# Optimization experiments

Hardware: AMD Instinct MI355X
Metric: run time of the kernel (lower is better)

Reference implementation:

```python
import jax, jax.numpy as jnp
import numpy as np

B, N, FEAT, D = 8, 2048, 64, 6
RADIUS, NSAMPLE, TOPK, NHEAD, NLAYER = 0.3, 64, 16, 8, 2
EPS = 1e-5


def _bn(x, p, axis=1):
    # eval-mode batchnorm; p rows = (gamma, beta, running_mean, running_var)
    g, b, m, v = p
    sh = [1] * x.ndim
    sh[axis] = -1
    rs = lambda t: t.reshape(sh)
    return (x - rs(m)) * (rs(g) / jnp.sqrt(rs(v) + EPS)) + rs(b)


def _ln(x, g, b):
    mu = jnp.mean(x, -1, keepdims=True)
    var = jnp.mean((x - mu) ** 2, -1, keepdims=True)
    return (x - mu) / jnp.sqrt(var + EPS) * g + b


def _mha(x, w_in, b_in, w_out, b_out):
    bsz, n, e = x.shape
    hd = e // NHEAD
    qkv = x @ w_in.T + b_in                      # [B,N,3E]
    q, k, v = jnp.split(qkv, 3, axis=-1)
    sp = lambda t: t.reshape(bsz, n, NHEAD, hd).transpose(0, 2, 1, 3)  # [B,H,N,hd]
    q, k, v = sp(q), sp(k), sp(v)
    att = jax.nn.softmax(jnp.einsum('bhnd,bhmd->bhnm', q, k) * (1.0 / hd ** 0.5), axis=-1)
    o = jnp.einsum('bhnm,bhmd->bhnd', att, v).transpose(0, 2, 1, 3).reshape(bsz, n, e)
    return o @ w_out.T + b_out


def _forward(sortvec, input, tl_win, tl_bin, tl_wout, tl_bout, tl_w1, tl_b1, tl_w2, tl_b2,
             tl_ln1g, tl_ln1b, tl_ln2g, tl_ln2b,
             fg_w0, fg_b0, fg_w1, fg_b1, fg_w2, fg_b2, fbn0, fbn1, fbn2,
             rc_w0, rc_b0, rc_w1, rc_b1, rc_w2, rc_b2, rbn0, rbn1, rbn2,
             fl_w0, fl_b0, fl_w1, fl_b1, lbn0, lbn1):
    b = sortvec.shape[0]
    n = sortvec.shape[-1]
    relu = jax.nn.relu

    # --- input self-attention (2 post-norm TransformerEncoder layers) ---
    x = sortvec[:, 0].transpose(0, 2, 1)         # [B,N,FEAT]
    for l in range(NLAYER):
        a = _mha(x, tl_win[l], tl_bin[l], tl_wout[l], tl_bout[l])
        x = _ln(x + a, tl_ln1g[l], tl_ln1b[l])
        f = relu(x @ tl_w1[l].T + tl_b1[l]) @ tl_w2[l].T + tl_b2[l]
        x = _ln(x + f, tl_ln2g[l], tl_ln2b[l])

    # --- feat_generator (RFFNet: Conv2d(FEAT,1) then 1x1 convs) + BN + relu ---
    s = jnp.einsum('cf,bnf->bcn', fg_w0, x) + fg_b0[:, None]   # [B,64,N]
    s = relu(_bn(s, fbn0))
    s = relu(_bn(jnp.einsum('co,bon->bcn', fg_w1, s) + fg_b1[:, None], fbn1))
    s = relu(_bn(jnp.einsum('co,bon->bcn', fg_w2, s) + fg_b2[:, None], fbn2))
    scores = s[:, 0]                              # [B,N]

    # --- top-k point selection ---
    _, idx = jax.lax.top_k(scores, TOPK)          # [B,K]
    all_points = input.transpose(0, 2, 1)         # [B,N,6]
    bidx = jnp.arange(b)[:, None]
    query = all_points[bidx, idx]                 # [B,K,6]

    # --- query_ball_point (PointNet++ style) ---
    xyz, qxyz = all_points[..., :3], query[..., :3]
    sqr = jnp.sum((qxyz[:, :, None, :] - xyz[:, None, :, :]) ** 2, -1)   # [B,K,N]
    gidx = jnp.where(sqr > RADIUS ** 2, n, jnp.arange(n)[None, None, :])
    gidx = jnp.sort(gidx, axis=-1)[..., :NSAMPLE]                        # [B,K,S]
    gidx = jnp.where(gidx == n, gidx[..., :1], gidx)
    radius_points = all_points[jnp.arange(b)[:, None, None], gidx]       # [B,K,S,6]
    grouped = jnp.concatenate([query[:, :, None, :], radius_points], axis=2)  # [B,K,S+1,6]

    # --- radius_cnn (Conv3d (1,S+1,6) then 1x1x1) + BN3d + relu ---
    r = jnp.einsum('cpd,bkpd->bck', rc_w0, grouped) + rc_b0[:, None]     # [B,128,K]
    r = relu(_bn(r, rbn0))
    r = relu(_bn(jnp.einsum('co,bok->bck', rc_w1, r) + rc_b1[:, None], rbn1))
    r = relu(_bn(jnp.einsum('co,bok->bck', rc_w2, r) + rc_b2[:, None], rbn2))  # [B,512,K]

    # --- flatten + Linear/BN1d/relu chain ---
    h = r.reshape(b, -1)                          # [B, 512*K]
    h = relu(_bn(h @ fl_w0.T + fl_b0, lbn0))
    h = relu(_bn(h @ fl_w1.T + fl_b1, lbn1))
    return h[..., None], idx                      # [B,512,1], [B,K]


def setup_inputs() -> dict:
    key = jax.random.key(0)
    ks = iter(jax.random.split(key, 80))
    rnd = lambda shape, s=0.02: jax.random.normal(next(ks), shape, jnp.float32) * s

    def bn_p(c):
        g = 1.0 + rnd((c,))
        bb = rnd((c,))
        m = rnd((c,))
        v = 1.0 + 0.1 * jnp.abs(rnd((c,), 1.0))
        return jnp.stack([g, bb, m, v])

    F = FEAT
    return dict(
        sortvec=jax.random.normal(next(ks), (B, 1, F, N), jnp.float32),
        input=jax.random.normal(next(ks), (B, D, N), jnp.float32),
        tl_win=rnd((NLAYER, 3 * F, F)), tl_bin=rnd((NLAYER, 3 * F)),
        tl_wout=rnd((NLAYER, F, F)), tl_bout=rnd((NLAYER, F)),
        tl_w1=rnd((NLAYER, 2048, F)), tl_b1=rnd((NLAYER, 2048)),
        tl_w2=rnd((NLAYER, F, 2048)), tl_b2=rnd((NLAYER, F)),
        tl_ln1g=jnp.ones((NLAYER, F)), tl_ln1b=jnp.zeros((NLAYER, F)),
        tl_ln2g=jnp.ones((NLAYER, F)), tl_ln2b=jnp.zeros((NLAYER, F)),
        fg_w0=rnd((64, F), 0.1), fg_b0=jnp.zeros((64,)),
        fg_w1=rnd((16, 64), 0.1), fg_b1=jnp.zeros((16,)),
        fg_w2=rnd((1, 16), 0.1), fg_b2=jnp.zeros((1,)),
        fbn0=bn_p(64), fbn1=bn_p(16), fbn2=bn_p(1),
        rc_w0=rnd((128, NSAMPLE + 1, D), 0.05), rc_b0=jnp.zeros((128,)),
        rc_w1=rnd((256, 128), 0.05), rc_b1=jnp.zeros((256,)),
        rc_w2=rnd((512, 256), 0.05), rc_b2=jnp.zeros((512,)),
        rbn0=bn_p(128), rbn1=bn_p(256), rbn2=bn_p(512),
        fl_w0=rnd((1024, 512 * TOPK), 0.02), fl_b0=jnp.zeros((1024,)),
        fl_w1=rnd((512, 1024), 0.02), fl_b1=jnp.zeros((512,)),
        lbn0=bn_p(1024), lbn1=bn_p(512),
    )


def reference(sortvec, input, tl_win, tl_bin, tl_wout, tl_bout, tl_w1, tl_b1, tl_w2, tl_b2,
              tl_ln1g, tl_ln1b, tl_ln2g, tl_ln2b,
              fg_w0, fg_b0, fg_w1, fg_b1, fg_w2, fg_b2, fbn0, fbn1, fbn2,
              rc_w0, rc_b0, rc_w1, rc_b1, rc_w2, rc_b2, rbn0, rbn1, rbn2,
              fl_w0, fl_b0, fl_w1, fl_b1, lbn0, lbn1):
    return _forward(sortvec, input, tl_win, tl_bin, tl_wout, tl_bout, tl_w1, tl_b1, tl_w2, tl_b2,
                    tl_ln1g, tl_ln1b, tl_ln2g, tl_ln2b,
                    fg_w0, fg_b0, fg_w1, fg_b1, fg_w2, fg_b2, fbn0, fbn1, fbn2,
                    rc_w0, rc_b0, rc_w1, rc_b1, rc_w2, rc_b2, rbn0, rbn1, rbn2,
                    fl_w0, fl_b0, fl_w1, fl_b1, lbn0, lbn1)
```

## Files before the change

kernel.cpp:

```cpp
#include <hip/hip_runtime.h>
#include <hip/hip_bf16.h>
#include <math.h>

#define BB 8
#define NN 2048
#define FF 64
#define DD 6
#define NSAMP 64
#define TOPK 16
#define NHEAD 8
#define HD 8
#define NLAYER 2
#define EPSF 1e-5f
#define R2 0.09f

typedef short short8 __attribute__((ext_vector_type(8)));
typedef float f32x4 __attribute__((ext_vector_type(4)));
typedef unsigned uint4v __attribute__((ext_vector_type(4)));
typedef unsigned int u32;

__device__ inline unsigned pk2(float x) {
  unsigned b = __float_as_uint(x);
  unsigned hi = (b + 0x7fffu + ((b >> 16) & 1u)) >> 16;
  float r = x - __uint_as_float(hi << 16);
  unsigned c = __float_as_uint(r);
  unsigned lo = (c + 0x7fffu + ((c >> 16) & 1u)) >> 16;
  return (hi << 16) | lo;
}

__device__ inline unsigned short bf16r(float x) {
  unsigned b = __float_as_uint(x);
  return (unsigned short)((b + 0x7fffu + ((b >> 16) & 1u)) >> 16);
}

__device__ __forceinline__ void gl16(const void* g, void* l) {
  __builtin_amdgcn_global_load_lds((const __attribute__((address_space(1))) u32*)g,
                                   (__attribute__((address_space(3))) u32*)l, 16, 0, 0);
}

__global__ void k_transpose(const float* __restrict__ sv, float* __restrict__ x) {
  int i = blockIdx.x * 256 + threadIdx.x;
  if (i >= BB * NN * FF) return;
  int f = i % FF;
  int n = (i / FF) % NN;
  int b = i / (FF * NN);
  x[i] = sv[(b * FF + f) * NN + n];
}

__global__ void k_wimg(const float* __restrict__ w1, const float* __restrict__ w2,
                       unsigned short* __restrict__ img) {
  int i = blockIdx.x * 256 + threadIdx.x;
  int e = i & 4095;
  int plane = (i >> 12) & 3;
  int chg = (i >> 14) & 31;
  int l = i >> 19;
  int r = e >> 6, sh = (e >> 3) & 7, inner = e & 7;
  int s = sh ^ (r & 7);
  float v;
  if (plane < 2) v = w1[((size_t)(l * 2048 + chg * 64 + r)) * 64 + s * 8 + inner];
  else           v = w2[((size_t)(l * 64 + r)) * 2048 + chg * 64 + s * 8 + inner];
  unsigned p = pk2(v);
  img[i] = (unsigned short)((plane & 1) ? (p & 0xffffu) : (p >> 16));
}

__global__ void k_qkv3(const float* __restrict__ x, const float* __restrict__ win,
                       const float* __restrict__ bin, float* __restrict__ qbuf,
                       uint4* __restrict__ kp4, uint4* __restrict__ vp4) {
  __shared__ float xs[64 * 68];
  __shared__ float ws[64 * 68];
  int row0 = blockIdx.x * 64, y = blockIdx.y, col0 = y * 64;
  int t = threadIdx.x;
  #pragma unroll
  for (int i = 0; i < 4; ++i) {
    int q = t + i * 256, r = q >> 4, c = (q & 15) * 4;
    *(float4*)(xs + r * 68 + c) = *(const float4*)(x + (size_t)(row0 + r) * 64 + c);
    *(float4*)(ws + r * 68 + c) = *(const float4*)(win + (size_t)(col0 + r) * 64 + c);
  }
  __syncthreads();
  int tx = t & 15, ty = t >> 4;
  float acc[4][4] = {};
  for (int f = 0; f < 64; f += 4) {
    float4 xv[4], wv[4];
    #pragma unroll
    for (int ri = 0; ri < 4; ++ri) xv[ri] = *(const float4*)(xs + (ty * 4 + ri) * 68 + f);
    #pragma unroll
    for (int ci = 0; ci < 4; ++ci) wv[ci] = *(const float4*)(ws + (tx + 16 * ci) * 68 + f);
    #pragma unroll
    for (int ri = 0; ri < 4; ++ri)
      #pragma unroll
      for (int ci = 0; ci < 4; ++ci)
        acc[ri][ci] += xv[ri].x * wv[ci].x + xv[ri].y * wv[ci].y +
                       xv[ri].z * wv[ci].z + xv[ri].w * wv[ci].w;
  }
  int b = row0 >> 11, n0 = row0 & (NN - 1);
  if (y == 0) {
    #pragma unroll
    for (int ri = 0; ri < 4; ++ri)
      #pragma unroll
      for (int ci = 0; ci < 4; ++ci) {
        int r = row0 + ty * 4 + ri, c = tx + 16 * ci;
        qbuf[(size_t)r * 64 + c] = acc[ri][ci] + bin[c];
      }
    return;
  }
  __syncthreads();
  unsigned short* l16 = (unsigned short*)xs;
  if (y == 1) {
    #pragma unroll
    for (int ri = 0; ri < 4; ++ri)
      #pragma unroll
      for (int ci = 0; ci < 4; ++ci) {
        int r = ty * 4 + ri, c = tx + 16 * ci;
        l16[r * 72 + c] = bf16r(acc[ri][ci] + bin[64 + c]);
      }
    __syncthreads();
    #pragma unroll
    for (int i = 0; i < 2; ++i) {
      int idx = t + i * 256;
      int h = idx >> 6, tok = idx & 63;
      uint4 v = *(const uint4*)(l16 + tok * 72 + h * 8);
      kp4[(size_t)(b * NHEAD + h) * NN + n0 + tok] = v;
    }
  } else {
    #pragma unroll
    for (int ri = 0; ri < 4; ++ri)
      #pragma unroll
      for (int ci = 0; ci < 4; ++ci) {
        int r = ty * 4 + ri, c = tx + 16 * ci;
        l16[c * 72 + r] = bf16r(acc[ri][ci] + bin[128 + c]);
      }
    __syncthreads();
    #pragma unroll
    for (int i = 0; i < 2; ++i) {
      int idx = t + i * 256;
      int c = idx >> 3, seg = idx & 7;
      uint4 v = *(const uint4*)(l16 + c * 72 + seg * 8);
      vp4[(size_t)(b * 64 + c) * (NN / 8) + (n0 >> 3) + seg] = v;
    }
  }
}

__global__ void __launch_bounds__(256, 8)
k_attn8(const float* __restrict__ q, const uint4* __restrict__ kp4,
        const unsigned* __restrict__ vp32, float* __restrict__ a) {
  __shared__ uint4 kb4[256];
  __shared__ __attribute__((aligned(16))) unsigned short vb16[9 * 264];
  int t = threadIdx.x;
  int lane = t & 63, w = t >> 6;
  int nIdx = lane & 15, lq = lane >> 4;
  int h = blockIdx.y, b = blockIdx.z;
  int qwb = blockIdx.x * 64 + w * 16;
  int bh = b * NHEAD + h;
  const float kf = 0.35355339059327373f * 1.4426950408889634f;
  short8 qF = {0, 0, 0, 0, 0, 0, 0, 0};
  if (lq == 0) {
    const float* qr = q + ((size_t)(b * NN + qwb + nIdx)) * 64 + h * HD;
    #pragma unroll
    for (int j = 0; j < 8; ++j) qF[j] = (short)bf16r(qr[j] * kf);
  }
  f32x4 acc = {0.f, 0.f, 0.f, 0.f};
  const uint4* kbase = kp4 + (size_t)bh * NN;
  const unsigned* vbase = vp32 + (size_t)bh * HD * (NN / 2);
  int vn = nIdx < 9 ? nIdx : 8;
  int voff = ((lq & 1) << 4) + ((lq >> 1) << 3);
  if (t < 132) ((unsigned*)(vb16 + 8 * 264))[t] = 0x3f803f80u;
  uint4 kreg = kbase[t];
  unsigned vreg[4];
  #pragma unroll
  for (int i = 0; i < 4; ++i) {
    int g = t + i * 256;
    vreg[i] = vbase[(g >> 7) * (NN / 2) + (g & 127)];
  }
  for (int kc = 0; kc < NN; kc += 256) {
    __syncthreads();
    kb4[t] = kreg;
    #pragma unroll
    for (int i = 0; i < 4; ++i) {
      int g = t + i * 256;
      ((unsigned*)vb16)[(g >> 7) * 132 + (g & 127)] = vreg[i];
    }
    __syncthreads();
    if (kc + 256 < NN) {
      kreg = kbase[kc + 256 + t];
      #pragma unroll
      for (int i = 0; i < 4; ++i) {
        int g = t + i * 256;
        vreg[i] = vbase[(g >> 7) * (NN / 2) + ((kc + 256) >> 1) + (g & 127)];
      }
    }
    for (int s = 0; s < 8; ++s) {
      int kb = s * 32;
      unsigned pk_[4];
      #pragma unroll
      for (int half = 0; half < 2; ++half) {
        int key = kb + half * 16 + nIdx;
        short8 aK = {0, 0, 0, 0, 0, 0, 0, 0};
        if (lq == 0) aK = *(const short8*)(kb4 + key);
        f32x4 c = {0.f, 0.f, 0.f, 0.f};
        c = __builtin_amdgcn_mfma_f32_16x16x32_bf16(aK, qF, c, 0, 0, 0);
        unsigned u0 = __float_as_uint(__builtin_amdgcn_exp2f(c[0]));
        unsigned u1 = __float_as_uint(__builtin_amdgcn_exp2f(c[1]));
        unsigned u2 = __float_as_uint(__builtin_amdgcn_exp2f(c[2]));
        unsigned u3 = __float_as_uint(__builtin_amdgcn_exp2f(c[3]));
        pk_[half * 2]     = (u0 >> 16) | (u1 & 0xffff0000u);
        pk_[half * 2 + 1] = (u2 >> 16) | (u3 & 0xffff0000u);
      }
      unsigned e0 = (unsigned)__shfl_xor((int)pk_[0], 16);
      unsigned e1 = (unsigned)__shfl_xor((int)pk_[1], 16);
      unsigned e2 = (unsigned)__shfl_xor((int)pk_[2], 16);
      unsigned e3 = (unsigned)__shfl_xor((int)pk_[3], 16);
      bool odd = (lq & 1);
      uint4v bw;
      bw[0] = odd ? e2 : pk_[0];
      bw[1] = odd ? e3 : pk_[1];
      bw[2] = odd ? pk_[2] : e0;
      bw[3] = odd ? pk_[3] : e1;
      short8 bP = *(short8*)&bw;
      short8 aV = *(const short8*)(vb16 + vn * 264 + kb + voff);
      acc = __builtin_amdgcn_mfma_f32_16x16x32_bf16(aV, bP, acc, 0, 0, 0);
    }
  }
  float lr = __shfl(acc[0], 32 + nIdx);
  if (lq < 2) {
    int row = qwb + nIdx;
    float4 o;
    o.x = acc[0] / lr; o.y = acc[1] / lr; o.z = acc[2] / lr; o.w = acc[3] / lr;
    *(float4*)(a + ((size_t)(b * NN + row)) * 64 + h * HD + lq * 4) = o;
  }
}

__global__ void k_proj2(const float* __restrict__ a, const float* __restrict__ wout,
                        const float* __restrict__ bout, const float* __restrict__ g,
                        const float* __restrict__ be, float* __restrict__ x) {
  __shared__ float xs[64 * 68];
  __shared__ float ws[64 * 68];
  int row0 = blockIdx.x * 64;
  int t = threadIdx.x;
  #pragma unroll
  for (int i = 0; i < 4; ++i) {
    int q = t + i * 256, r = q >> 4, c = (q & 15) * 4;
    *(float4*)(xs + r * 68 + c) = *(const float4*)(a + (size_t)(row0 + r) * 64 + c);
    *(float4*)(ws + r * 68 + c) = *(const float4*)(wout + r * 64 + c);
  }
  __syncthreads();
  int tx = t & 15, ty = t >> 4;
  float acc[4][4] = {};
  for (int f = 0; f < 64; f += 4) {
    float4 xv[4], wv[4];
    #pragma unroll
    for (int ri = 0; ri < 4; ++ri) xv[ri] = *(const float4*)(xs + (ty * 4 + ri) * 68 + f);
    #pragma unroll
    for (int ci = 0; ci < 4; ++ci) wv[ci] = *(const float4*)(ws + (tx + 16 * ci) * 68 + f);
    #pragma unroll
    for (int ri = 0; ri < 4; ++ri)
      #pragma unroll
      for (int ci = 0; ci < 4; ++ci)
        acc[ri][ci] += xv[ri].x * wv[ci].x + xv[ri].y * wv[ci].y +
                       xv[ri].z * wv[ci].z + xv[ri].w * wv[ci].w;
  }
  #pragma unroll
  for (int ri = 0; ri < 4; ++ri) {
    int rl = ty * 4 + ri;
    float val[4], s = 0.f, sq = 0.f;
    #pragma unroll
    for (int ci = 0; ci < 4; ++ci) {
      int c = tx + 16 * ci;
      val[ci] = x[(size_t)(row0 + rl) * 64 + c] + bout[c] + acc[ri][ci];
      s += val[ci]; sq += val[ci] * val[ci];
    }
    #pragma unroll
    for (int off = 1; off < 16; off <<= 1) { s += __shfl_xor(s, off); sq += __shfl_xor(sq, off); }
    float mean = s * (1.f / 64.f);
    float var = sq * (1.f / 64.f) - mean * mean;
    float rstd = rsqrtf(var + EPSF);
    #pragma unroll
    for (int ci = 0; ci < 4; ++ci) {
      int c = tx + 16 * ci;
      x[(size_t)(row0 + rl) * 64 + c] = (val[ci] - mean) * rstd * g[c] + be[c];
    }
  }
}

__global__ void __launch_bounds__(256, 2)
k_ffn7(const float* __restrict__ x, const char* __restrict__ img,
       const float* __restrict__ b1, float* __restrict__ part) {
  __shared__ __attribute__((aligned(16))) char W1b[2][16384];
  __shared__ __attribute__((aligned(16))) char W2b[16384];
  __shared__ __attribute__((aligned(16))) unsigned short hpl[2][128 * 64];
  int row0 = blockIdx.x * 128;
  int ks = blockIdx.y, kc = ks * 512;
  int t = threadIdx.x, lane = t & 63, wv = t >> 6;
  int lm = lane & 15, lq = lane >> 4;
  const char* ibase = img + (size_t)ks * 8 * 32768;

  short8 axh[2][2], axl[2][2];
  #pragma unroll
  for (int m = 0; m < 2; ++m)
    #pragma unroll
    for (int kbi = 0; kbi < 2; ++kbi) {
      const float* xr = x + (size_t)(row0 + m * 64 + wv * 16 + lm) * 64 + kbi * 32 + lq * 8;
      #pragma unroll
      for (int j = 0; j < 8; ++j) {
        unsigned p = pk2(xr[j]);
        axh[m][kbi][j] = (short)(p >> 16);
        axl[m][kbi][j] = (short)(p & 0xffffu);
      }
    }
  float bv[8][4];
  #pragma unroll
  for (int ch = 0; ch < 8; ++ch)
    #pragma unroll
    for (int tn = 0; tn < 4; ++tn)
      bv[ch][tn] = b1[kc + ch * 64 + tn * 16 + lm];
  asm volatile("s_waitcnt vmcnt(0)" ::: "memory");
  __builtin_amdgcn_sched_barrier(0);
  #pragma unroll
  for (int i = 0; i < 4; ++i)
    gl16(ibase + i * 4096 + t * 16, &W1b[0][i * 4096 + t * 16]);

  f32x4 acc[2][4];
  #pragma unroll
  for (int m = 0; m < 2; ++m)
    #pragma unroll
    for (int tn = 0; tn < 4; ++tn) acc[m][tn] = (f32x4){0.f, 0.f, 0.f, 0.f};

  #pragma unroll
  for (int ch = 0; ch < 8; ++ch) {
    const int p = ch & 1;
    const char* cbase = ibase + ch * 32768;
    #pragma unroll
    for (int i = 0; i < 4; ++i)
      gl16(cbase + 16384 + i * 4096 + t * 16, &W2b[i * 4096 + t * 16]);
    if (ch < 7) {
      #pragma unroll
      for (int i = 0; i < 4; ++i)
        gl16(cbase + 32768 + i * 4096 + t * 16, &W1b[p ^ 1][i * 4096 + t * 16]);
    }
    if (ch < 7) { asm volatile("s_waitcnt vmcnt(8)" ::: "memory"); }
    else        { asm volatile("s_waitcnt vmcnt(4)" ::: "memory"); }
    __builtin_amdgcn_sched_barrier(0);
    __builtin_amdgcn_s_barrier();
    __builtin_amdgcn_sched_barrier(0);
    const char* P0h = W1b[p];
    const char* P0l = W1b[p] + 8192;
    f32x4 h4[2][4];
    #pragma unroll
    for (int m = 0; m < 2; ++m)
      #pragma unroll
      for (int tn = 0; tn < 4; ++tn) h4[m][tn] = (f32x4){0.f, 0.f, 0.f, 0.f};
    #pragma unroll
    for (int kbi = 0; kbi < 2; ++kbi) {
      int sw = (((kbi * 4 + lq) ^ (lm & 7)) << 4);
      #pragma unroll
      for (int tn = 0; tn < 4; ++tn) {
        int brow = tn * 16 + lm;
        short8 bhi = *(const short8*)(P0h + brow * 128 + sw);
        short8 blo = *(const short8*)(P0l + brow * 128 + sw);
        #pragma unroll
        for (int m = 0; m < 2; ++m) {
          h4[m][tn] = __builtin_amdgcn_mfma_f32_16x16x32_bf16(axh[m][kbi], bhi, h4[m][tn], 0, 0, 0);
          h4[m][tn] = __builtin_amdgcn_mfma_f32_16x16x32_bf16(axh[m][kbi], blo, h4[m][tn], 0, 0, 0);
          h4[m][tn] = __builtin_amdgcn_mfma_f32_16x16x32_bf16(axl[m][kbi], bhi, h4[m][tn], 0, 0, 0);
        }
      }
    }
    #pragma unroll
    for (int m = 0; m < 2; ++m)
      #pragma unroll
      for (int tn = 0; tn < 4; ++tn)
        #pragma unroll
        for (int r = 0; r < 4; ++r) {
          float hv = fmaxf(h4[m][tn][r] + bv[ch][tn], 0.f);
          unsigned u = __float_as_uint(hv);
          float resid = hv - __uint_as_float(u & 0xffff0000u);
          unsigned c2 = __float_as_uint(resid);
          int hrow = m * 64 + wv * 16 + lq * 4 + r, hcol = tn * 16 + lm;
          int off = hrow * 128 + (((hcol >> 3) ^ (hrow & 7)) << 4) + ((hcol & 7) << 1);
          *(unsigned short*)((char*)hpl[0] + off) = (unsigned short)(u >> 16);
          *(unsigned short*)((char*)hpl[1] + off) =
              (unsigned short)((c2 + 0x7fffu + ((c2 >> 16) & 1u)) >> 16);
        }
    if (ch < 7) { asm volatile("s_waitcnt vmcnt(4)" ::: "memory"); }
    else        { asm volatile("s_waitcnt vmcnt(0)" ::: "memory"); }
    __builtin_amdgcn_sched_barrier(0);
    __builtin_amdgcn_s_barrier();
    __builtin_amdgcn_sched_barrier(0);
    const char* P1h = W2b;
    const char* P1l = W2b + 8192;
    #pragma unroll
    for (int kbi = 0; kbi < 2; ++kbi) {
      short8 a2h[2], a2l[2];
      #pragma unroll
      for (int m = 0; m < 2; ++m) {
        int arow = m * 64 + wv * 16 + lm;
        int swa = (((kbi * 4 + lq) ^ (arow & 7)) << 4);
        a2h[m] = *(const short8*)((const char*)hpl[0] + arow * 128 + swa);
        a2l[m] = *(const short8*)((const char*)hpl[1] + arow * 128 + swa);
      }
      int swb = (((kbi * 4 + lq) ^ (lm & 7)) << 4);
      #pragma unroll
      for (int tn = 0; tn < 4; ++tn) {
        int brow = tn * 16 + lm;
        short8 bhi = *(const short8*)(P1h + brow * 128 + swb);
        short8 blo = *(const short8*)(P1l + brow * 128 + swb);
        #pragma unroll
        for (int m = 0; m < 2; ++m) {
          acc[m][tn] = __builtin_amdgcn_mfma_f32_16x16x32_bf16(a2h[m], bhi, acc[m][tn], 0, 0, 0);
          acc[m][tn] = __builtin_amdgcn_mfma_f32_16x16x32_bf16(a2h[m], blo, acc[m][tn], 0, 0, 0);
          acc[m][tn] = __builtin_amdgcn_mfma_f32_16x16x32_bf16(a2l[m], bhi, acc[m][tn], 0, 0, 0);
        }
      }
    }
    __builtin_amdgcn_s_barrier();
    __builtin_amdgcn_sched_barrier(0);
  }
  float* fb = (float*)hpl;
  #pragma unroll
  for (int m = 0; m < 2; ++m)
    #pragma unroll
    for (int tn = 0; tn < 4; ++tn)
      #pragma unroll
      for (int r = 0; r < 4; ++r) {
        int row = m * 64 + wv * 16 + lq * 4 + r;
        int col = (tn * 16 + lm) ^ ((row & 7) << 2);
        fb[row * 64 + col] = acc[m][tn][r];
      }
  __syncthreads();
  float* pb = part + (size_t)ks * (BB * NN * 64);
  #pragma unroll
  for (int i = 0; i < 8; ++i) {
    int idx = t * 4 + i * 1024;
    int row = idx >> 6, c0 = idx & 63;
    int c0s = c0 ^ ((row & 7) << 2);
    float4 v = *(const float4*)(fb + row * 64 + c0s);
    *(float4*)(pb + (size_t)(row0 + row) * 64 + c0) = v;
  }
}

__global__ void k_ffn_ln(const float* __restrict__ part, const float* __restrict__ b2,
                         const float* __restrict__ g, const float* __restrict__ be,
                         float* __restrict__ x) {
  int row = blockIdx.x * 4 + (threadIdx.x >> 6);
  int j = threadIdx.x & 63;
  size_t o = (size_t)row * 64 + j;
  const size_t S = (size_t)BB * NN * 64;
  float val = x[o] + b2[j] + ((part[o] + part[o + S]) + (part[o + 2 * S] + part[o + 3 * S]));
  float s = val;
  for (int off = 32; off; off >>= 1) s += __shfl_xor(s, off);
  s *= (1.f / 64.f);
  float d = val - s;
  float v = d * d;
  for (int off = 32; off; off >>= 1) v += __shfl_xor(v, off);
  v *= (1.f / 64.f);
  x[o] = d * rsqrtf(v + EPSF) * g[j] + be[j];
}

__global__ void k_fg2(const float* __restrict__ x,
                      const float* __restrict__ w0, const float* __restrict__ b0, const float* __restrict__ bn0,
                      const float* __restrict__ w1, const float* __restrict__ b1, const float* __restrict__ bn1,
                      const float* __restrict__ w2, const float* __restrict__ b2, const float* __restrict__ bn2,
                      float* __restrict__ scores) {
  __shared__ float xs[64 * 68];
  __shared__ float ws[64 * 68];
  __shared__ float s0s[64 * 68];
  __shared__ float s1s[64 * 20];
  int row0 = blockIdx.x * 64;
  int t = threadIdx.x;
  #pragma unroll
  for (int i = 0; i < 4; ++i) {
    int q = t + i * 256, r = q >> 4, c = (q & 15) * 4;
    *(float4*)(xs + r * 68 + c) = *(const float4*)(x + (size_t)(row0 + r) * 64 + c);
    *(float4*)(ws + r * 68 + c) = *(const float4*)(w0 + r * 64 + c);
  }
  __syncthreads();
  int tx = t & 15, ty = t >> 4;
  float acc[4][4] = {};
  for (int f = 0; f < 64; f += 4) {
    float4 xv[4], wv[4];
    #pragma unroll
    for (int ri = 0; ri < 4; ++ri) xv[ri] = *(const float4*)(xs + (ty * 4 + ri) * 68 + f);
    #pragma unroll
    for (int ci = 0; ci < 4; ++ci) wv[ci] = *(const float4*)(ws + (tx + 16 * ci) * 68 + f);
    #pragma unroll
    for (int ri = 0; ri < 4; ++ri)
      #pragma unroll
      for (int ci = 0; ci < 4; ++ci)
        acc[ri][ci] += xv[ri].x * wv[ci].x + xv[ri].y * wv[ci].y +
                       xv[ri].z * wv[ci].z + xv[ri].w * wv[ci].w;
  }
  #pragma unroll
  for (int ri = 0; ri < 4; ++ri)
    #pragma unroll
    for (int ci = 0; ci < 4; ++ci) {
      int c = tx + 16 * ci;
      float sc = bn0[c] * rsqrtf(bn0[192 + c] + EPSF);
      float v = (acc[ri][ci] + b0[c] - bn0[128 + c]) * sc + bn0[64 + c];
      s0s[(ty * 4 + ri) * 68 + c] = fmaxf(v, 0.f);
    }
  __syncthreads();
  {
    int rl = t & 63, j0 = t >> 6;
    #pragma unroll
    for (int i = 0; i < 4; ++i) {
      int j = j0 + 4 * i;
      float s = b1[j];
      const float* wr = w1 + j * 64;
      #pragma unroll 16
      for (int c = 0; c < 64; ++c) s += s0s[rl * 68 + c] * wr[c];
      float sc = bn1[j] * rsqrtf(bn1[48 + j] + EPSF);
      s = (s - bn1[32 + j]) * sc + bn1[16 + j];
      s1s[rl * 20 + j] = fmaxf(s, 0.f);
    }
  }
  __syncthreads();
  if (t < 64) {
    float s = b2[0];
    #pragma unroll
    for (int o = 0; o < 16; ++o) s += s1s[t * 20 + o] * w2[o];
    float sc = bn2[0] * rsqrtf(bn2[3] + EPSF);
    s = (s - bn2[2]) * sc + bn2[1];
    scores[row0 + t] = fmaxf(s, 0.f);
  }
}

__global__ void k_topk2(const float* __restrict__ scores, int* __restrict__ idx,
                        float* __restrict__ out_idx) {
  int b = blockIdx.x, t = threadIdx.x;
  float v[8];
  int base = b * NN;
  #pragma unroll
  for (int u = 0; u < 8; ++u) v[u] = scores[base + t + 256 * u];
  __shared__ float wvs[4];
  __shared__ int wis[4];
  __shared__ int winner;
  unsigned taken = 0;
  for (int r = 0; r < TOPK; ++r) {
    float best = -1e30f; int bi = 1 << 30;
    #pragma unroll
    for (int u = 0; u < 8; ++u) {
      if (!((taken >> u) & 1)) {
        float vv = v[u]; int ii = t + 256 * u;
        if (vv > best || (vv == best && ii < bi)) { best = vv; bi = ii; }
      }
    }
    for (int off = 32; off; off >>= 1) {
      float ov = __shfl_xor(best, off);
      int oi = __shfl_xor(bi, off);
      if (ov > best || (ov == best && oi < bi)) { best = ov; bi = oi; }
    }
    if ((t & 63) == 0) { wvs[t >> 6] = best; wis[t >> 6] = bi; }
    __syncthreads();
    if (t == 0) {
      float B = wvs[0]; int I = wis[0];
      #pragma unroll
      for (int q = 1; q < 4; ++q)
        if (wvs[q] > B || (wvs[q] == B && wis[q] < I)) { B = wvs[q]; I = wis[q]; }
      winner = I;
      idx[b * TOPK + r] = I;
      out_idx[b * TOPK + r] = (float)I;
    }
    __syncthreads();
    int w = winner;
    if ((w & 255) == t) taken |= 1u << (w >> 8);
  }
}

__global__ void __launch_bounds__(512)
k_group(const float* __restrict__ inp, const int* __restrict__ idx,
        const float* __restrict__ w0, const float* __restrict__ b0, const float* __restrict__ bn0,
        const float* __restrict__ w1, const float* __restrict__ b1, const float* __restrict__ bn1,
        const float* __restrict__ w2, const float* __restrict__ b2, const float* __restrict__ bn2,
        float* __restrict__ r2g) {
  __shared__ int swave[8 * 64];
  __shared__ int scnt[8];
  __shared__ int gidx[NSAMP];
  __shared__ __attribute__((aligned(16))) float gsh[65 * DD];
  __shared__ __attribute__((aligned(16))) float r0[128];
  __shared__ __attribute__((aligned(16))) float r1[256];
  int k = blockIdx.x, b = blockIdx.y;
  int t = threadIdx.x;
  int lane = t & 63, w = t >> 6;
  int qn = idx[b * TOPK + k];
  const float* px = inp + (size_t)b * DD * NN;
  float qx = px[qn], qy = px[NN + qn], qz = px[2 * NN + qn];
  {
    int cnt = 0;
    #pragma unroll
    for (int i = 0; i < 4; ++i) {
      int n = w * 256 + i * 64 + lane;
      float dx = px[n] - qx, dy = px[NN + n] - qy, dz = px[2 * NN + n] - qz;
      bool flag = (dx * dx + dy * dy + dz * dz <= R2);
      unsigned long long m = __ballot(flag);
      int pos = cnt + __popcll(m & ((1ull << lane) - 1ull));
      if (flag && pos < NSAMP) swave[w * 64 + pos] = n;
      cnt += (int)__popcll(m);
    }
    if (lane == 0) scnt[w] = cnt < NSAMP ? cnt : NSAMP;
  }
  __syncthreads();
  if (t < NSAMP) {
    int run = 0, val = -1;
    #pragma unroll
    for (int ww = 0; ww < 8; ++ww) {
      int c = scnt[ww];
      int loc = t - run;
      if (loc >= 0 && loc < c) val = swave[ww * 64 + loc];
      run += c;
    }
    gidx[t] = val;
  }
  __syncthreads();
  if (t < NSAMP) {
    int g0 = gidx[0];
    int gt = gidx[t];
    gidx[t] = (gt < 0) ? g0 : gt;
  }
  __syncthreads();
  if (t < 65 * DD) {
    int p = t / DD, d = t - p * DD;
    int n = (p == 0) ? qn : gidx[p - 1];
    gsh[t] = px[d * NN + n];
  }
  __syncthreads();
  {
    int c = t >> 2, part = t & 3;
    const float2* wr = (const float2*)(w0 + c * 390 + part * 98);
    const float2* gr = (const float2*)(gsh + part * 98);
    int n2 = (part == 3) ? 48 : 49;
    float s = 0.f;
    #pragma unroll 7
    for (int i = 0; i < n2; ++i) {
      float2 a = gr[i], ww = wr[i];
      s += a.x * ww.x + a.y * ww.y;
    }
    s += __shfl_xor(s, 1);
    s += __shfl_xor(s, 2);
    if (part == 0) {
      s += b0[c];
      float sc = bn0[c] * rsqrtf(bn0[384 + c] + EPSF);
      s = (s - bn0[256 + c]) * sc + bn0[128 + c];
      r0[c] = fmaxf(s, 0.f);
    }
  }
  __syncthreads();
  {
    int c = t >> 1, part = t & 1;
    const float4* wr = (const float4*)(w1 + c * 128 + part * 64);
    const float4* rr = (const float4*)(r0 + part * 64);
    float s0 = 0.f, s1 = 0.f, s2 = 0.f, s3 = 0.f;
    #pragma unroll 8
    for (int o = 0; o < 16; ++o) {
      float4 a = rr[o], ww = wr[o];
      s0 += a.x * ww.x; s1 += a.y * ww.y; s2 += a.z * ww.z; s3 += a.w * ww.w;
    }
    float s = (s0 + s1) + (s2 + s3);
    s += __shfl_xor(s, 1);
    if (part == 0) {
      s += b1[c];
      float sc = bn1[c] * rsqrtf(bn1[768 + c] + EPSF);
      s = (s - bn1[512 + c]) * sc + bn1[256 + c];
      r1[c] = fmaxf(s, 0.f);
    }
  }
  __syncthreads();
  {
    int c = t;
    const float4* wr = (const float4*)(w2 + c * 256);
    const float4* rr = (const float4*)r1;
    float s0 = 0.f, s1 = 0.f, s2 = 0.f, s3 = 0.f;
    #pragma unroll 8
    for (int o = 0; o < 64; ++o) {
      float4 a = rr[o], ww = wr[o];
      s0 += a.x * ww.x; s1 += a.y * ww.y; s2 += a.z * ww.z; s3 += a.w * ww.w;
    }
    float s = (s0 + s1) + (s2 + s3) + b2[c];
    float sc = bn2[c] * rsqrtf(bn2[1536 + c] + EPSF);
    s = (s - bn2[1024 + c]) * sc + bn2[512 + c];
    r2g[b * 8192 + c * TOPK + k] = fmaxf(s, 0.f);
  }
}

__global__ void __launch_bounds__(256)
k_fl2(const float* __restrict__ hin, const float* __restrict__ w,
      float* __restrict__ part) {
  __shared__ float hs[8 * 1032];
  int j0 = blockIdx.x * 16;
  int kc = blockIdx.y * 1024;
  int t = threadIdx.x;
  int jj = t >> 4, l = t & 15;
  #pragma unroll
  for (int i = 0; i < 8; ++i) {
    int idx = t + i * 256;
    int b = idx >> 8, off = (idx & 255) * 4;
    *(float4*)(hs + b * 1032 + off) = *(const float4*)(hin + (size_t)b * 8192 + kc + off);
  }
  __syncthreads();
  const float* wr = w + (size_t)(j0 + jj) * 8192 + kc;
  float acc[8] = {};
  #pragma unroll
  for (int k = 0; k < 16; ++k) {
    float4 wv = *(const float4*)(wr + l * 4 + k * 64);
    #pragma unroll
    for (int b = 0; b < 8; ++b) {
      float4 hv = *(const float4*)(hs + b * 1032 + l * 4 + k * 64);
      acc[b] += wv.x * hv.x + wv.y * hv.y + wv.z * hv.z + wv.w * hv.w;
    }
  }
  #pragma unroll
  for (int b = 0; b < 8; ++b) {
    #pragma unroll
    for (int off = 1; off < 16; off <<= 1) acc[b] += __shfl_xor(acc[b], off);
  }
  if (l == 0) {
    #pragma unroll
    for (int b = 0; b < 8; ++b)
      part[((size_t)blockIdx.y * 8 + b) * 1024 + j0 + jj] = acc[b];
  }
}

__global__ void k_flc(const float* __restrict__ part, const float* __restrict__ bias,
                      const float* __restrict__ bn, float* __restrict__ hout) {
  int i = blockIdx.x * 256 + threadIdx.x;
  int b = i >> 10, j = i & 1023;
  float s = bias[j];
  #pragma unroll
  for (int ks = 0; ks < 8; ++ks) s += part[((size_t)ks * 8 + b) * 1024 + j];
  float sc = bn[j] * rsqrtf(bn[3 * 1024 + j] + EPSF);
  s = (s - bn[2 * 1024 + j]) * sc + bn[1024 + j];
  hout[i] = fmaxf(s, 0.f);
}

__global__ void k_fl(const float* __restrict__ hin, const float* __restrict__ w,
                     const float* __restrict__ bias, const float* __restrict__ bn,
                     float* __restrict__ hout, int IN, int OUT) {
  int blk = blockIdx.x;
  int b = blk / OUT, j = blk % OUT;
  int lane = threadIdx.x;
  const float* hr = hin + (size_t)b * IN;
  const float* wr = w + (size_t)j * IN;
  float s = 0.f;
  for (int i = lane; i < IN; i += 64) s += hr[i] * wr[i];
  for (int o = 32; o; o >>= 1) s += __shfl_xor(s, o);
  if (lane == 0) {
    s += bias[j];
    float sc = bn[j] * rsqrtf(bn[3 * OUT + j] + EPSF);
    s = (s - bn[2 * OUT + j]) * sc + bn[OUT + j];
    hout[b * OUT + j] = fmaxf(s, 0.f);
  }
}

extern "C" void kernel_launch(void* const* d_in, const int* in_sizes, int n_in,
                              void* d_out, int out_size, void* d_ws, size_t ws_size,
                              hipStream_t stream) {
  const float* sv      = (const float*)d_in[0];
  const float* inp     = (const float*)d_in[1];
  const float* tl_win  = (const float*)d_in[2];
  const float* tl_bin  = (const float*)d_in[3];
  const float* tl_wout = (const float*)d_in[4];
  const float* tl_bout = (const float*)d_in[5];
  const float* tl_w1   = (const float*)d_in[6];
  const float* tl_b1   = (const float*)d_in[7];
  const float* tl_w2   = (const float*)d_in[8];
  const float* tl_b2   = (const float*)d_in[9];
  const float* tl_ln1g = (const float*)d_in[10];
  const float* tl_ln1b = (const float*)d_in[11];
  const float* tl_ln2g = (const float*)d_in[12];
  const float* tl_ln2b = (const float*)d_in[13];
  const float* fg_w0   = (const float*)d_in[14];
  const float* fg_b0   = (const float*)d_in[15];
  const float* fg_w1   = (const float*)d_in[16];
  const float* fg_b1   = (const float*)d_in[17];
  const float* fg_w2   = (const float*)d_in[18];
  const float* fg_b2   = (const float*)d_in[19];
  const float* fbn0    = (const float*)d_in[20];
  const float* fbn1    = (const float*)d_in[21];
  const float* fbn2    = (const float*)d_in[22];
  const float* rc_w0   = (const float*)d_in[23];
  const float* rc_b0   = (const float*)d_in[24];
  const float* rc_w1   = (const float*)d_in[25];
  const float* rc_b1   = (const float*)d_in[26];
  const float* rc_w2   = (const float*)d_in[27];
  const float* rc_b2   = (const float*)d_in[28];
  const float* rbn0    = (const float*)d_in[29];
  const float* rbn1    = (const float*)d_in[30];
  const float* rbn2    = (const float*)d_in[31];
  const float* fl_w0   = (const float*)d_in[32];
  const float* fl_b0   = (const float*)d_in[33];
  const float* fl_w1   = (const float*)d_in[34];
  const float* fl_b1   = (const float*)d_in[35];
  const float* lbn0    = (const float*)d_in[36];
  const float* lbn1    = (const float*)d_in[37];
  (void)in_sizes; (void)n_in; (void)out_size; (void)ws_size;

  float* wsp = (float*)d_ws;
  float* x      = wsp;
  float* qkv    = x + BB * NN * FF;
  float* a      = qkv + BB * NN * 192;
  float* scores = a + BB * NN * FF;
  int*   idxb   = (int*)(scores + BB * NN);
  float* r2g    = (float*)(idxb + BB * TOPK);
  float* h1g    = r2g + BB * 8192;
  unsigned short* img = (unsigned short*)(h1g + BB * 1024);
  float* qbuf = qkv;
  unsigned short* kp = (unsigned short*)(qkv + BB * NN * FF);
  unsigned short* vp = kp + (size_t)BB * NHEAD * NN * HD;
  float* part = qkv;

  float* out = (float*)d_out;

  k_transpose<<<(BB * NN * FF) / 256, 256, 0, stream>>>(sv, x);
  k_wimg<<<(NLAYER * 32 * 4 * 4096) / 256, 256, 0, stream>>>(tl_w1, tl_w2, img);

  for (int l = 0; l < NLAYER; ++l) {
    k_qkv3<<<dim3(BB * NN / 64, 3), 256, 0, stream>>>(x, tl_win + l * 192 * FF,
                                                      tl_bin + l * 192, qbuf,
                                                      (uint4*)kp, (uint4*)vp);
    k_attn8<<<dim3(NN / 64, NHEAD, BB), 256, 0, stream>>>(qbuf, (const uint4*)kp,
                                                          (const unsigned*)vp, a);
    k_proj2<<<BB * NN / 64, 256, 0, stream>>>(a, tl_wout + l * FF * FF, tl_bout + l * FF,
                                              tl_ln1g + l * FF, tl_ln1b + l * FF, x);
    k_ffn7<<<dim3(BB * NN / 128, 4), 256, 0, stream>>>(x, (const char*)(img + (size_t)l * 524288),
                                                       tl_b1 + l * 2048, part);
    k_ffn_ln<<<BB * NN / 4, 256, 0, stream>>>(part, tl_b2 + l * FF,
                                              tl_ln2g + l * FF, tl_ln2b + l * FF, x);
  }

  k_fg2<<<BB * NN / 64, 256, 0, stream>>>(x, fg_w0, fg_b0, fbn0, fg_w1, fg_b1, fbn1,
                                          fg_w2, fg_b2, fbn2, scores);
  k_topk2<<<BB, 256, 0, stream>>>(scores, idxb, out + BB * 512);
  k_group<<<dim3(TOPK, BB), 512, 0, stream>>>(inp, idxb, rc_w0, rc_b0, rbn0,
                                              rc_w1, rc_b1, rbn1, rc_w2, rc_b2, rbn2, r2g);
  k_fl2<<<dim3(64, 8), 256, 0, stream>>>(r2g, fl_w0, part);
  k_flc<<<32, 256, 0, stream>>>(part, fl_b0, lbn0, h1g);
  k_fl<<<BB * 512, 64, 0, stream>>>(h1g, fl_w1, fl_b1, lbn1, out, 1024, 512);
}
```

Baseline: 447.8 us.

## Tune attention MFMA priority and bf16 packing; split-K batched final FC layer

The attention kernel now raises wave priority around its MFMA instructions. It also converts the exp2 results to bf16 with the hardware v_cvt_pk_bf16_f32 instruction, which rounds, where the old code truncated with bit masks. The last fully connected layer used one 64-thread block per (batch, output) pair and reread the weights for each batch. It is replaced by a split-K kernel that loads each weight row once for all 8 batches, plus a small reduction and batchnorm kernel. The exp conversion now rounds instead of truncating, which changes numerics slightly, and the new path adds one kernel launch.

Result: no change. 442.2 us (-1.3%).

```diff
diff --git a/kernel.cpp b/kernel.cpp
--- a/kernel.cpp
+++ b/kernel.cpp
@@ -141,7 +141,7 @@
 }
 
 __global__ void __launch_bounds__(256, 8)
-k_attn8(const float* __restrict__ q, const uint4* __restrict__ kp4,
+k_attn9(const float* __restrict__ q, const uint4* __restrict__ kp4,
         const unsigned* __restrict__ vp32, float* __restrict__ a) {
   __shared__ uint4 kb4[256];
   __shared__ __attribute__((aligned(16))) unsigned short vb16[9 * 264];
@@ -197,13 +197,18 @@
         short8 aK = {0, 0, 0, 0, 0, 0, 0, 0};
         if (lq == 0) aK = *(const short8*)(kb4 + key);
         f32x4 c = {0.f, 0.f, 0.f, 0.f};
+        __builtin_amdgcn_s_setprio(1);
         c = __builtin_amdgcn_mfma_f32_16x16x32_bf16(aK, qF, c, 0, 0, 0);
-        unsigned u0 = __float_as_uint(__builtin_amdgcn_exp2f(c[0]));
-        unsigned u1 = __float_as_uint(__builtin_amdgcn_exp2f(c[1]));
-        unsigned u2 = __float_as_uint(__builtin_amdgcn_exp2f(c[2]));
-        unsigned u3 = __float_as_uint(__builtin_amdgcn_exp2f(c[3]));
-        pk_[half * 2]     = (u0 >> 16) | (u1 & 0xffff0000u);
-        pk_[half * 2 + 1] = (u2 >> 16) | (u3 & 0xffff0000u);
+        __builtin_amdgcn_s_setprio(0);
+        float p0 = __builtin_amdgcn_exp2f(c[0]);
+        float p1 = __builtin_amdgcn_exp2f(c[1]);
+        float p2 = __builtin_amdgcn_exp2f(c[2]);
+        float p3 = __builtin_amdgcn_exp2f(c[3]);
+        unsigned r0, r1;
+        asm("v_cvt_pk_bf16_f32 %0, %1, %2" : "=v"(r0) : "v"(p0), "v"(p1));
+        asm("v_cvt_pk_bf16_f32 %0, %1, %2" : "=v"(r1) : "v"(p2), "v"(p3));
+        pk_[half * 2]     = r0;
+        pk_[half * 2 + 1] = r1;
       }
       unsigned e0 = (unsigned)__shfl_xor((int)pk_[0], 16);
       unsigned e1 = (unsigned)__shfl_xor((int)pk_[1], 16);
@@ -217,7 +222,9 @@
       bw[3] = odd ? pk_[3] : e1;
       short8 bP = *(short8*)&bw;
       short8 aV = *(const short8*)(vb16 + vn * 264 + kb + voff);
+      __builtin_amdgcn_s_setprio(1);
       acc = __builtin_amdgcn_mfma_f32_16x16x32_bf16(aV, bP, acc, 0, 0, 0);
+      __builtin_amdgcn_s_setprio(0);
     }
   }
   float lr = __shfl(acc[0], 32 + nIdx);
@@ -730,23 +737,54 @@
   hout[i] = fmaxf(s, 0.f);
 }
 
-__global__ void k_fl(const float* __restrict__ hin, const float* __restrict__ w,
-                     const float* __restrict__ bias, const float* __restrict__ bn,
-                     float* __restrict__ hout, int IN, int OUT) {
-  int blk = blockIdx.x;
-  int b = blk / OUT, j = blk % OUT;
-  int lane = threadIdx.x;
-  const float* hr = hin + (size_t)b * IN;
-  const float* wr = w + (size_t)j * IN;
-  float s = 0.f;
-  for (int i = lane; i < IN; i += 64) s += hr[i] * wr[i];
-  for (int o = 32; o; o >>= 1) s += __shfl_xor(s, o);
-  if (lane == 0) {
-    s += bias[j];
-    float sc = bn[j] * rsqrtf(bn[3 * OUT + j] + EPSF);
-    s = (s - bn[2 * OUT + j]) * sc + bn[OUT + j];
-    hout[b * OUT + j] = fmaxf(s, 0.f);
-  }
+__global__ void __launch_bounds__(256)
+k_fl3(const float* __restrict__ hin, const float* __restrict__ w,
+      float* __restrict__ part) {
+  __shared__ float hs[8 * 264];
+  int j0 = blockIdx.x * 16;
+  int kc = blockIdx.y * 256;
+  int t = threadIdx.x;
+  int jj = t >> 4, l = t & 15;
+  #pragma unroll
+  for (int i = 0; i < 2; ++i) {
+    int idx = t + i * 256;
+    int b = idx >> 6, off = (idx & 63) * 4;
+    *(float4*)(hs + b * 264 + off) = *(const float4*)(hin + (size_t)b * 1024 + kc + off);
+  }
+  __syncthreads();
+  const float* wr = w + (size_t)(j0 + jj) * 1024 + kc;
+  float acc[8] = {};
+  #pragma unroll
+  for (int k = 0; k < 4; ++k) {
+    float4 wv = *(const float4*)(wr + l * 4 + k * 64);
+    #pragma unroll
+    for (int b = 0; b < 8; ++b) {
+      float4 hv = *(const float4*)(hs + b * 264 + l * 4 + k * 64);
+      acc[b] += wv.x * hv.x + wv.y * hv.y + wv.z * hv.z + wv.w * hv.w;
+    }
+  }
+  #pragma unroll
+  for (int b = 0; b < 8; ++b) {
+    #pragma unroll
+    for (int off = 1; off < 16; off <<= 1) acc[b] += __shfl_xor(acc[b], off);
+  }
+  if (l == 0) {
+    #pragma unroll
+    for (int b = 0; b < 8; ++b)
+      part[((size_t)blockIdx.y * 8 + b) * 512 + j0 + jj] = acc[b];
+  }
+}
+
+__global__ void k_flc2(const float* __restrict__ part, const float* __restrict__ bias,
+                       const float* __restrict__ bn, float* __restrict__ hout) {
+  int i = blockIdx.x * 256 + threadIdx.x;
+  int b = i >> 9, j = i & 511;
+  float s = bias[j];
+  #pragma unroll
+  for (int ks = 0; ks < 4; ++ks) s += part[((size_t)ks * 8 + b) * 512 + j];
+  float sc = bn[j] * rsqrtf(bn[3 * 512 + j] + EPSF);
+  s = (s - bn[2 * 512 + j]) * sc + bn[512 + j];
+  hout[i] = fmaxf(s, 0.f);
 }
 
 extern "C" void kernel_launch(void* const* d_in, const int* in_sizes, int n_in,
@@ -805,6 +843,7 @@
   unsigned short* kp = (unsigned short*)(qkv + BB * NN * FF);
   unsigned short* vp = kp + (size_t)BB * NHEAD * NN * HD;
   float* part = qkv;
+  float* part2 = qkv + 65536;
 
   float* out = (float*)d_out;
 
@@ -815,7 +854,7 @@
     k_qkv3<<<dim3(BB * NN / 64, 3), 256, 0, stream>>>(x, tl_win + l * 192 * FF,
                                                       tl_bin + l * 192, qbuf,
                                                       (uint4*)kp, (uint4*)vp);
-    k_attn8<<<dim3(NN / 64, NHEAD, BB), 256, 0, stream>>>(qbuf, (const uint4*)kp,
+    k_attn9<<<dim3(NN / 64, NHEAD, BB), 256, 0, stream>>>(qbuf, (const uint4*)kp,
                                                           (const unsigned*)vp, a);
     k_proj2<<<BB * NN / 64, 256, 0, stream>>>(a, tl_wout + l * FF * FF, tl_bout + l * FF,
                                               tl_ln1g + l * FF, tl_ln1b + l * FF, x);
@@ -832,5 +871,6 @@
                                               rc_w1, rc_b1, rbn1, rc_w2, rc_b2, rbn2, r2g);
   k_fl2<<<dim3(64, 8), 256, 0, stream>>>(r2g, fl_w0, part);
   k_flc<<<32, 256, 0, stream>>>(part, fl_b0, lbn0, h1g);
-  k_fl<<<BB * 512, 64, 0, stream>>>(h1g, fl_w1, fl_b1, lbn1, out, 1024, 512);
-}
+  k_fl3<<<dim3(32, 4), 256, 0, stream>>>(h1g, fl_w1, part2);
+  k_flc2<<<16, 256, 0, stream>>>(part2, fl_b1, lbn1, out);
+}
```
